# Kernel tuning notes

Hardware: AMD Instinct MI355X
Metric: run time of the kernel (lower is better)

Reference implementation:

```python
import jax, jax.numpy as jnp
import numpy as np

D_MODEL = 96
D_INNER = 192   # ssm_ratio * d_model
R = 6           # dt_rank = ceil(96/16)
DH = 32         # d_inner // dt_rank (per-head dim)
K = 4           # scan directions
N = 16          # d_state
EPS = 1e-5


def setup_inputs() -> dict:
    key = jax.random.key(0)
    ks = jax.random.split(key, 10)
    B, H, W = 8, 64, 64
    f = lambda k, s, sc: jax.random.normal(k, s, jnp.float32) * sc
    return dict(
        x=jax.random.normal(ks[0], (B, H, W, D_MODEL), jnp.float32),
        w_in=f(ks[1], (D_MODEL, D_INNER), 0.02),
        w_conv=f(ks[2], (3, 3, 1, D_INNER), 0.1),      # depthwise HWIO
        b_conv=f(ks[3], (D_INNER,), 0.1),
        x_proj_weight=f(ks[4], (K, R + 2 * N, D_INNER), 0.02),
        A_logs=f(ks[5], (K, R), 0.5),
        Ds=jnp.ones((K, R, DH), jnp.float32),
        dt_bias=0.1 * jax.random.uniform(ks[6], (K, R), jnp.float32),
        ln_g=jnp.ones((D_INNER,), jnp.float32),
        ln_b=jnp.zeros((D_INNER,), jnp.float32),
        w_out=f(ks[7], (D_INNER, D_MODEL), 0.02),
    )


def _cross_scan(x):
    # x: (B,H,W,C) -> (B,L,4,C): [row-major, col-major, rev row, rev col]
    B, H, W, C = x.shape
    x0 = x.reshape(B, H * W, C)
    x1 = jnp.transpose(x, (0, 2, 1, 3)).reshape(B, H * W, C)
    return jnp.stack([x0, x1, x0[:, ::-1], x1[:, ::-1]], axis=2)


def _cross_merge(ys, H, W):
    # ys: (B,L,4,C) -> (B,L,C) summed after undoing each scan order
    B, L, _, C = ys.shape
    y_row = ys[:, :, 0] + ys[:, :, 2][:, ::-1]
    y_col = ys[:, :, 1] + ys[:, :, 3][:, ::-1]
    y_col = jnp.transpose(y_col.reshape(B, W, H, C), (0, 2, 1, 3)).reshape(B, L, C)
    return y_row + y_col


def _selective_scan(us, dts, As, Bs, Cs, Dsr, dtb):
    # us:(B,L,KR,DH) dts:(B,L,KR) As:(KR,) Bs,Cs:(B,L,K,N) Dsr:(KR,DH) dtb:(KR,)
    dt = jax.nn.softplus(dts + dtb)                 # (B,L,KR)
    decay = jnp.exp(dt * As)                        # (B,L,KR)
    xu = dt[..., None] * us                         # (B,L,KR,DH)
    Bh = jnp.repeat(Bs, R, axis=2)                  # (B,L,KR,N) head h -> group h//R
    Ch = jnp.repeat(Cs, R, axis=2)
    B_, L, KR, _ = us.shape
    tfirst = lambda a: jnp.moveaxis(a, 1, 0)

    def step(h, inp):
        dec, xu_t, b_t, c_t = inp                   # (B,KR),(B,KR,DH),(B,KR,N),(B,KR,N)
        h = dec[:, :, None, None] * h + xu_t[..., None] * b_t[:, :, None, :]
        y = jnp.einsum('bkdn,bkn->bkd', h, c_t)
        return h, y

    h0 = jnp.zeros((B_, KR, DH, N), us.dtype)
    _, ys = jax.lax.scan(step, h0, (tfirst(decay), tfirst(xu), tfirst(Bh), tfirst(Ch)))
    ys = jnp.moveaxis(ys, 0, 1)                     # (B,L,KR,DH)
    return ys + us * Dsr                            # skip term D*u


def reference(x, w_in, w_conv, b_conv, x_proj_weight, A_logs, Ds, dt_bias, ln_g, ln_b, w_out):
    B, H, W, _ = x.shape
    L = H * W
    xi = x @ w_in                                   # in_proj (no bias)
    xi = jax.lax.conv_general_dilated(
        xi, w_conv, (1, 1), 'SAME', feature_group_count=D_INNER,
        dimension_numbers=('NHWC', 'HWIO', 'NHWC')) + b_conv
    xi = jax.nn.silu(xi)
    xs = _cross_scan(xi)                            # (B,L,4,D_INNER)
    x_dbl = jnp.einsum('blkd,kcd->blkc', xs, x_proj_weight)
    dts = x_dbl[..., :R].reshape(B, L, K * R)
    Bs = x_dbl[..., R:R + N]                        # (B,L,K,N)
    Cs = x_dbl[..., R + N:]
    us = xs.reshape(B, L, K * R, DH)
    As = -jnp.exp(A_logs.astype(jnp.float32)).reshape(K * R)
    Dsr = Ds.reshape(K * R, DH)
    dtb = dt_bias.reshape(K * R)
    ys = _selective_scan(us, dts, As, Bs, Cs, Dsr, dtb)   # (B,L,KR,DH)
    y = _cross_merge(ys.reshape(B, L, K, R * DH), H, W)   # (B,L,D_INNER)
    mu = y.mean(-1, keepdims=True)
    var = ((y - mu) ** 2).mean(-1, keepdims=True)
    y = (y - mu) / jnp.sqrt(var + EPS) * ln_g + ln_b
    y = y.reshape(B, H, W, D_INNER)
    return y @ w_out                                # out_proj (no bias)
```

## Files before the change

kernel.cpp:

```cpp
#include <hip/hip_runtime.h>
#include <hip/hip_bf16.h>

#define BB 8
#define LL 4096
#define DM 96
#define DI 192
#define RRR 6
#define DHH 32
#define KKK 4
#define NNN 16
#define KRR 24
#define NCH 64
#define TT 64
#define XKC 160

__device__ __forceinline__ float softplus_f(float x){
    float ax = fabsf(x);
    return fmaxf(x, 0.f) + __logf(1.f + __expf(-ax));
}
__device__ __forceinline__ float silu_f(float x){ return x / (1.f + __expf(-x)); }

__device__ __forceinline__ int loc_of(int k, int t){
    int tt = (k >= 2) ? (LL - 1 - t) : t;
    if (k & 1) return ((tt & 63) << 6) | (tt >> 6);
    return tt;
}

__global__ void k0p(const float* __restrict__ W, const float* __restrict__ g,
                    const float* __restrict__ bta, const float* __restrict__ w_out,
                    float* __restrict__ Wp, float* __restrict__ wg, float* __restrict__ sgbw){
    int i = blockIdx.x * 256 + threadIdx.x;
    if (i < DI * XKC){
        int d = i / XKC, kc = i % XKC; int k = kc / 40, nc = kc % 40;
        float v = 0.f;
        if (nc < 6) v = W[(k * 38 + nc) * DI + d];
        else if (nc >= 8) v = W[(k * 38 + (nc - 2)) * DI + d];
        Wp[i] = v;
    } else if (i < DI * XKC + DI * DM){
        int j = i - DI * XKC; int c = j / DM;
        wg[j] = w_out[j] * g[c];
    } else if (i < DI * XKC + DI * DM + DM){
        int m = i - (DI * XKC + DI * DM);
        float s = 0.f, t = 0.f;
        for (int c = 0; c < DI; ++c){
            float w = w_out[c * DM + m];
            s = fmaf(g[c], w, s);
            t = fmaf(bta[c], w, t);
        }
        sgbw[m] = s; sgbw[DM + m] = t;
    }
}

__global__ __launch_bounds__(384) void k1_inproj(const float* __restrict__ x,
                                                 const float* __restrict__ w_in,
                                                 float* __restrict__ xw){
    __shared__ float xT[DM][68];
    int pix0 = blockIdx.x * 64;
    for (int i = threadIdx.x; i < 64 * DM; i += 384){
        int c = i % DM, p = i / DM;
        xT[c][p] = x[(size_t)(pix0 + p) * DM + c];
    }
    __syncthreads();
    int cg = threadIdx.x % 48, pg = threadIdx.x / 48;
    int p0 = pg * 8;
    float4 acc[8];
    #pragma unroll
    for (int i = 0; i < 8; ++i) acc[i] = make_float4(0.f, 0.f, 0.f, 0.f);
    const float* wcol = w_in + cg * 4;
    for (int d = 0; d < DM; ++d){
        float4 w4 = *(const float4*)(wcol + d * DI);
        float4 xa = *(const float4*)(&xT[d][p0]);
        float4 xb = *(const float4*)(&xT[d][p0 + 4]);
        float xs[8] = {xa.x, xa.y, xa.z, xa.w, xb.x, xb.y, xb.z, xb.w};
        #pragma unroll
        for (int pi = 0; pi < 8; ++pi){
            acc[pi].x = fmaf(xs[pi], w4.x, acc[pi].x);
            acc[pi].y = fmaf(xs[pi], w4.y, acc[pi].y);
            acc[pi].z = fmaf(xs[pi], w4.z, acc[pi].z);
            acc[pi].w = fmaf(xs[pi], w4.w, acc[pi].w);
        }
    }
    #pragma unroll
    for (int pi = 0; pi < 8; ++pi)
        *(float4*)(xw + (size_t)(pix0 + p0 + pi) * DI + cg * 4) = acc[pi];
}

__global__ void k2_conv(const float* __restrict__ xw, const float* __restrict__ wc,
                        const float* __restrict__ bc, float* __restrict__ xi){
    int gid = blockIdx.x * 256 + threadIdx.x;
    int c4 = gid % 48; int pix = gid / 48;
    int b = pix >> 12; int l = pix & 4095; int h = l >> 6; int w = l & 63;
    int c = c4 * 4;
    float4 acc = *(const float4*)(bc + c);
    #pragma unroll
    for (int dh = 0; dh < 3; ++dh){
        int hh = h + dh - 1; if ((unsigned)hh >= 64u) continue;
        #pragma unroll
        for (int dw = 0; dw < 3; ++dw){
            int ww2 = w + dw - 1; if ((unsigned)ww2 >= 64u) continue;
            float4 tap = *(const float4*)(xw + (size_t)((b << 12) + (hh << 6) + ww2) * DI + c);
            float4 wv  = *(const float4*)(wc + (dh * 3 + dw) * DI + c);
            acc.x = fmaf(tap.x, wv.x, acc.x);
            acc.y = fmaf(tap.y, wv.y, acc.y);
            acc.z = fmaf(tap.z, wv.z, acc.z);
            acc.w = fmaf(tap.w, wv.w, acc.w);
        }
    }
    acc.x = silu_f(acc.x); acc.y = silu_f(acc.y); acc.z = silu_f(acc.z); acc.w = silu_f(acc.w);
    *(float4*)(xi + (size_t)pix * DI + c) = acc;
}

__global__ __launch_bounds__(320) void k3_proj(const float* __restrict__ xi,
                                               const float* __restrict__ Wp,
                                               float* __restrict__ xdbl){
    __shared__ float xT[DI][68];
    int pix0 = blockIdx.x * 64;
    for (int i = threadIdx.x; i < 64 * DI; i += 320){
        int c = i % DI, p = i / DI;
        xT[c][p] = xi[(size_t)(pix0 + p) * DI + c];
    }
    __syncthreads();
    int kg = threadIdx.x % 40, pg = threadIdx.x / 40;
    int p0 = pg * 8;
    float4 acc[8];
    #pragma unroll
    for (int i = 0; i < 8; ++i) acc[i] = make_float4(0.f, 0.f, 0.f, 0.f);
    const float* wcol = Wp + kg * 4;
    for (int d = 0; d < DI; ++d){
        float4 w4 = *(const float4*)(wcol + d * XKC);
        float4 xa = *(const float4*)(&xT[d][p0]);
        float4 xb = *(const float4*)(&xT[d][p0 + 4]);
        float xs[8] = {xa.x, xa.y, xa.z, xa.w, xb.x, xb.y, xb.z, xb.w};
        #pragma unroll
        for (int pi = 0; pi < 8; ++pi){
            acc[pi].x = fmaf(xs[pi], w4.x, acc[pi].x);
            acc[pi].y = fmaf(xs[pi], w4.y, acc[pi].y);
            acc[pi].z = fmaf(xs[pi], w4.z, acc[pi].z);
            acc[pi].w = fmaf(xs[pi], w4.w, acc[pi].w);
        }
    }
    #pragma unroll
    for (int pi = 0; pi < 8; ++pi)
        *(float4*)(xdbl + (size_t)(pix0 + p0 + pi) * XKC + kg * 4) = acc[pi];
}

__global__ __launch_bounds__(192) void k4a(const float* __restrict__ xi, const float* __restrict__ xdbl,
                    const float* __restrict__ A_logs, const float* __restrict__ dt_bias,
                    float* __restrict__ Pb, float* __restrict__ Sb){
    int chunk = blockIdx.x, k = blockIdx.y, b = blockIdx.z;
    int r = threadIdx.x >> 5, d = threadIdx.x & 31;
    int kr = k * RRR + r;
    float A = -__expf(A_logs[kr]);
    float dtb = dt_bias[kr];
    float h[NNN];
    #pragma unroll
    for (int n = 0; n < NNN; ++n) h[n] = 0.f;
    float P = 1.f;
    const float* xd = xdbl + ((size_t)b << 12) * XKC + k * 40;
    const float* xib = xi + ((size_t)b << 12) * DI + r * DHH + d;
    #pragma unroll 2
    for (int tt = 0; tt < TT; ++tt){
        int t = chunk * TT + tt;
        int loc = loc_of(k, t);
        const float* row = xd + (size_t)loc * XKC;
        float dt = softplus_f(row[r] + dtb);
        float dec = __expf(dt * A);
        float u = xib[(size_t)loc * DI];
        float xu = dt * u;
        P *= dec;
        float Bv[NNN];
        *(float4*)(Bv + 0)  = *(const float4*)(row + 8);
        *(float4*)(Bv + 4)  = *(const float4*)(row + 12);
        *(float4*)(Bv + 8)  = *(const float4*)(row + 16);
        *(float4*)(Bv + 12) = *(const float4*)(row + 20);
        #pragma unroll
        for (int n = 0; n < NNN; ++n) h[n] = fmaf(dec, h[n], xu * Bv[n]);
    }
    size_t sb = (((size_t)(b * KRR + kr) * NCH + chunk) * DHH + d) * NNN;
    #pragma unroll
    for (int n = 0; n < NNN; ++n) Sb[sb + n] = h[n];
    if (d == 0) Pb[(size_t)(b * KRR + kr) * NCH + chunk] = P;
}

__global__ __launch_bounds__(512) void k4b(const float* __restrict__ Pb, float* __restrict__ Sb){
    int scan = blockIdx.x;
    int tid = threadIdx.x;
    size_t base = (size_t)scan * NCH * 512 + tid;
    const float* Pp = Pb + (size_t)scan * NCH;
    float s[NCH];
    #pragma unroll
    for (int c = 0; c < NCH; ++c) s[c] = Sb[base + (size_t)c * 512];
    float hb = 0.f;
    #pragma unroll
    for (int c = 0; c < NCH; ++c){
        float nv = fmaf(Pp[c], hb, s[c]);
        Sb[base + (size_t)c * 512] = hb;
        hb = nv;
    }
}

__global__ __launch_bounds__(192) void k4c(const float* __restrict__ xi, const float* __restrict__ xdbl,
                    const float* __restrict__ A_logs, const float* __restrict__ dt_bias,
                    const float* __restrict__ Ds, const float* __restrict__ Sb,
                    __hip_bfloat16* __restrict__ ybuf){
    int chunk = blockIdx.x, k = blockIdx.y, b = blockIdx.z;
    int r = threadIdx.x >> 5, d = threadIdx.x & 31;
    int kr = k * RRR + r;
    float A = -__expf(A_logs[kr]);
    float dtb = dt_bias[kr];
    float Dv = Ds[kr * DHH + d];
    float h[NNN];
    size_t sb = (((size_t)(b * KRR + kr) * NCH + chunk) * DHH + d) * NNN;
    #pragma unroll
    for (int n = 0; n < NNN; ++n) h[n] = Sb[sb + n];
    const float* xd = xdbl + ((size_t)b << 12) * XKC + k * 40;
    const float* xib = xi + ((size_t)b << 12) * DI + r * DHH + d;
    __hip_bfloat16* yb = ybuf + (size_t)(k * BB + b) * LL * DI + r * DHH + d;
    #pragma unroll 2
    for (int tt = 0; tt < TT; ++tt){
        int t = chunk * TT + tt;
        int loc = loc_of(k, t);
        const float* row = xd + (size_t)loc * XKC;
        float dt = softplus_f(row[r] + dtb);
        float dec = __expf(dt * A);
        float u = xib[(size_t)loc * DI];
        float xu = dt * u;
        float Bv[NNN], Cv[NNN];
        *(float4*)(Bv + 0)  = *(const float4*)(row + 8);
        *(float4*)(Bv + 4)  = *(const float4*)(row + 12);
        *(float4*)(Bv + 8)  = *(const float4*)(row + 16);
        *(float4*)(Bv + 12) = *(const float4*)(row + 20);
        *(float4*)(Cv + 0)  = *(const float4*)(row + 24);
        *(float4*)(Cv + 4)  = *(const float4*)(row + 28);
        *(float4*)(Cv + 8)  = *(const float4*)(row + 32);
        *(float4*)(Cv + 12) = *(const float4*)(row + 36);
        float y = 0.f;
        #pragma unroll
        for (int n = 0; n < NNN; ++n){
            h[n] = fmaf(dec, h[n], xu * Bv[n]);
            y = fmaf(h[n], Cv[n], y);
        }
        y = fmaf(u, Dv, y);
        yb[(size_t)loc * DI] = __float2bfloat16(y);
    }
}

__global__ __launch_bounds__(256) void k5_out(const __hip_bfloat16* __restrict__ ybuf,
                       const float* __restrict__ wg, const float* __restrict__ sgbw,
                       float* __restrict__ out){
    __shared__ float yT[DI][36];
    __shared__ float rsL[32], rmL[32];
    int pix0 = blockIdx.x * 32;
    int b = pix0 >> 12;
    int l0 = pix0 & 4095;
    const size_t kstride = (size_t)BB * LL * DI;
    for (int i = threadIdx.x; i < 32 * DI; i += 256){
        int c = i % DI, p = i / DI;
        size_t off = (size_t)b * LL * DI + (size_t)(l0 + p) * DI + c;
        float s = __bfloat162float(ybuf[off])
                + __bfloat162float(ybuf[off + kstride])
                + __bfloat162float(ybuf[off + 2 * kstride])
                + __bfloat162float(ybuf[off + 3 * kstride]);
        yT[c][p] = s;
    }
    __syncthreads();
    {
        int p = threadIdx.x >> 3, cg = threadIdx.x & 7;
        float s = 0.f, s2 = 0.f;
        for (int c = cg; c < DI; c += 8){ float v = yT[c][p]; s += v; s2 = fmaf(v, v, s2); }
        s += __shfl_xor(s, 1, 64); s2 += __shfl_xor(s2, 1, 64);
        s += __shfl_xor(s, 2, 64); s2 += __shfl_xor(s2, 2, 64);
        s += __shfl_xor(s, 4, 64); s2 += __shfl_xor(s2, 4, 64);
        if (cg == 0){
            float mu = s * (1.f / DI);
            float var = s2 * (1.f / DI) - mu * mu;
            float rs = rsqrtf(var + 1e-5f);
            rsL[p] = rs; rmL[p] = rs * mu;
        }
    }
    __syncthreads();
    if (threadIdx.x < 192){
        int mg = threadIdx.x % 24, pg = threadIdx.x / 24;
        int p0 = pg * 4;
        float4 acc[4];
        #pragma unroll
        for (int i = 0; i < 4; ++i) acc[i] = make_float4(0.f, 0.f, 0.f, 0.f);
        const float* wcol = wg + mg * 4;
        for (int c = 0; c < DI; ++c){
            float4 w4 = *(const float4*)(wcol + c * DM);
            float4 yv = *(const float4*)(&yT[c][p0]);
            float ys[4] = {yv.x, yv.y, yv.z, yv.w};
            #pragma unroll
            for (int pi = 0; pi < 4; ++pi){
                acc[pi].x = fmaf(ys[pi], w4.x, acc[pi].x);
                acc[pi].y = fmaf(ys[pi], w4.y, acc[pi].y);
                acc[pi].z = fmaf(ys[pi], w4.z, acc[pi].z);
                acc[pi].w = fmaf(ys[pi], w4.w, acc[pi].w);
            }
        }
        float4 sg4 = *(const float4*)(sgbw + mg * 4);
        float4 bw4 = *(const float4*)(sgbw + DM + mg * 4);
        #pragma unroll
        for (int pi = 0; pi < 4; ++pi){
            float rs = rsL[p0 + pi], rm = rmL[p0 + pi];
            float4 o;
            o.x = fmaf(acc[pi].x, rs, fmaf(-rm, sg4.x, bw4.x));
            o.y = fmaf(acc[pi].y, rs, fmaf(-rm, sg4.y, bw4.y));
            o.z = fmaf(acc[pi].z, rs, fmaf(-rm, sg4.z, bw4.z));
            o.w = fmaf(acc[pi].w, rs, fmaf(-rm, sg4.w, bw4.w));
            *(float4*)(out + (size_t)(pix0 + p0 + pi) * DM + mg * 4) = o;
        }
    }
}

extern "C" void kernel_launch(void* const* d_in, const int* in_sizes, int n_in,
                              void* d_out, int out_size, void* d_ws, size_t ws_size,
                              hipStream_t stream){
    const float* x      = (const float*)d_in[0];
    const float* w_in   = (const float*)d_in[1];
    const float* w_conv = (const float*)d_in[2];
    const float* b_conv = (const float*)d_in[3];
    const float* xproj  = (const float*)d_in[4];
    const float* A_logs = (const float*)d_in[5];
    const float* Ds     = (const float*)d_in[6];
    const float* dtbias = (const float*)d_in[7];
    const float* ln_g   = (const float*)d_in[8];
    const float* ln_b   = (const float*)d_in[9];
    const float* w_out  = (const float*)d_in[10];
    float* out = (float*)d_out;

    float* ws   = (float*)d_ws;
    float* xi   = ws;
    float* xdbl = xi + 6291456;
    float* Pb   = xdbl + 5242880;
    float* Sb   = Pb + 16384;
    float* Wp   = Sb + 6291456;
    float* wg   = Wp + 30720;
    float* sgbw = wg + 18432;
    float* big  = sgbw + 192;
    float* xw   = big;
    __hip_bfloat16* ybuf = (__hip_bfloat16*)big;

    k0p<<<193, 256, 0, stream>>>(xproj, ln_g, ln_b, w_out, Wp, wg, sgbw);
    k1_inproj<<<512, 384, 0, stream>>>(x, w_in, xw);
    k2_conv<<<6144, 256, 0, stream>>>(xw, w_conv, b_conv, xi);
    k3_proj<<<512, 320, 0, stream>>>(xi, Wp, xdbl);
    k4a<<<dim3(NCH, KKK, BB), 192, 0, stream>>>(xi, xdbl, A_logs, dtbias, Pb, Sb);
    k4b<<<192, 512, 0, stream>>>(Pb, Sb);
    k4c<<<dim3(NCH, KKK, BB), 192, 0, stream>>>(xi, xdbl, A_logs, dtbias, Ds, Sb, ybuf);
    k5_out<<<1024, 256, 0, stream>>>(ybuf, wg, sgbw, out);
}
```

Baseline: 304.7 us.

## Lay out scan inputs in per-direction sequence order and precompute dt/decay

The conv kernel now also writes a transposed copy of the activations, so column-major directions can be read contiguously. The projection kernel writes per-direction records in scan order and precomputes softplus(dt) and exp(dt*A) once, instead of in both scan passes. The scan kernels then stream through the records and activations with linear strides and no index remapping, and the merge undoes the orderings when reading. In exchange there is an extra full activation write and a larger workspace.

```diff
diff --git a/kernel.cpp b/kernel.cpp
--- a/kernel.cpp
+++ b/kernel.cpp
@@ -12,7 +12,7 @@
 #define KRR 24
 #define NCH 64
 #define TT 64
-#define XKC 160
+#define RST 48
 
 __device__ __forceinline__ float softplus_f(float x){
     float ax = fabsf(x);
@@ -20,27 +20,22 @@
 }
 __device__ __forceinline__ float silu_f(float x){ return x / (1.f + __expf(-x)); }
 
-__device__ __forceinline__ int loc_of(int k, int t){
-    int tt = (k >= 2) ? (LL - 1 - t) : t;
-    if (k & 1) return ((tt & 63) << 6) | (tt >> 6);
-    return tt;
-}
-
 __global__ void k0p(const float* __restrict__ W, const float* __restrict__ g,
                     const float* __restrict__ bta, const float* __restrict__ w_out,
-                    float* __restrict__ Wp, float* __restrict__ wg, float* __restrict__ sgbw){
+                    float* __restrict__ WpR, float* __restrict__ wg, float* __restrict__ sgbw){
     int i = blockIdx.x * 256 + threadIdx.x;
-    if (i < DI * XKC){
-        int d = i / XKC, kc = i % XKC; int k = kc / 40, nc = kc % 40;
+    if (i < DI * 160){
+        int d = i / 160, cc = i % 160; int gq = cc / 40, nc = cc % 40;
+        int dir = (gq == 0) ? 0 : (gq == 1) ? 2 : (gq == 2) ? 1 : 3;
         float v = 0.f;
-        if (nc < 6) v = W[(k * 38 + nc) * DI + d];
-        else if (nc >= 8) v = W[(k * 38 + (nc - 2)) * DI + d];
-        Wp[i] = v;
-    } else if (i < DI * XKC + DI * DM){
-        int j = i - DI * XKC; int c = j / DM;
+        if (nc < 6) v = W[(dir * 38 + nc) * DI + d];
+        else if (nc >= 8) v = W[(dir * 38 + (nc - 2)) * DI + d];
+        WpR[i] = v;
+    } else if (i < DI * 160 + DI * DM){
+        int j = i - DI * 160; int c = j / DM;
         wg[j] = w_out[j] * g[c];
-    } else if (i < DI * XKC + DI * DM + DM){
-        int m = i - (DI * XKC + DI * DM);
+    } else if (i < DI * 160 + DI * DM + DM){
+        int m = i - (DI * 160 + DI * DM);
         float s = 0.f, t = 0.f;
         for (int c = 0; c < DI; ++c){
             float w = w_out[c * DM + m];
@@ -86,7 +81,8 @@
 }
 
 __global__ void k2_conv(const float* __restrict__ xw, const float* __restrict__ wc,
-                        const float* __restrict__ bc, float* __restrict__ xi){
+                        const float* __restrict__ bc, float* __restrict__ xi,
+                        float* __restrict__ xiT){
     int gid = blockIdx.x * 256 + threadIdx.x;
     int c4 = gid % 48; int pix = gid / 48;
     int b = pix >> 12; int l = pix & 4095; int h = l >> 6; int w = l & 63;
@@ -108,73 +104,114 @@
     }
     acc.x = silu_f(acc.x); acc.y = silu_f(acc.y); acc.z = silu_f(acc.z); acc.w = silu_f(acc.w);
     *(float4*)(xi + (size_t)pix * DI + c) = acc;
-}
-
-__global__ __launch_bounds__(320) void k3_proj(const float* __restrict__ xi,
-                                               const float* __restrict__ Wp,
-                                               float* __restrict__ xdbl){
-    __shared__ float xT[DI][68];
-    int pix0 = blockIdx.x * 64;
+    int lT = ((l & 63) << 6) | (l >> 6);
+    *(float4*)(xiT + (size_t)((b << 12) + lT) * DI + c) = acc;
+}
+
+__global__ __launch_bounds__(320) void k3seq(const float* __restrict__ xi,
+                                             const float* __restrict__ xiT,
+                                             const float* __restrict__ WpR,
+                                             const float* __restrict__ A_logs,
+                                             const float* __restrict__ dtb,
+                                             float* __restrict__ rec){
+    __shared__ float xT[DI][65];
+    int pass = blockIdx.y, b = blockIdx.z;
+    const float* src = (pass ? xiT : xi) + (((size_t)b) << 12) * DI;
+    int p0blk = blockIdx.x * 64;
     for (int i = threadIdx.x; i < 64 * DI; i += 320){
         int c = i % DI, p = i / DI;
-        xT[c][p] = xi[(size_t)(pix0 + p) * DI + c];
+        xT[c][p] = src[(size_t)(p0blk + p) * DI + c];
     }
     __syncthreads();
-    int kg = threadIdx.x % 40, pg = threadIdx.x / 40;
-    int p0 = pg * 8;
-    float4 acc[8];
-    #pragma unroll
-    for (int i = 0; i < 8; ++i) acc[i] = make_float4(0.f, 0.f, 0.f, 0.f);
-    const float* wcol = Wp + kg * 4;
+    int kg = threadIdx.x % 20, pg = threadIdx.x / 20;
+    int p0 = pg * 4;
+    float4 acc[4];
+    #pragma unroll
+    for (int i = 0; i < 4; ++i) acc[i] = make_float4(0.f, 0.f, 0.f, 0.f);
+    const float* wcol = WpR + pass * 80 + kg * 4;
     for (int d = 0; d < DI; ++d){
-        float4 w4 = *(const float4*)(wcol + d * XKC);
-        float4 xa = *(const float4*)(&xT[d][p0]);
-        float4 xb = *(const float4*)(&xT[d][p0 + 4]);
-        float xs[8] = {xa.x, xa.y, xa.z, xa.w, xb.x, xb.y, xb.z, xb.w};
-        #pragma unroll
-        for (int pi = 0; pi < 8; ++pi){
+        float4 w4 = *(const float4*)(wcol + d * 160);
+        float4 xv = *(const float4*)(&xT[d][p0]);
+        float xs[4] = {xv.x, xv.y, xv.z, xv.w};
+        #pragma unroll
+        for (int pi = 0; pi < 4; ++pi){
             acc[pi].x = fmaf(xs[pi], w4.x, acc[pi].x);
             acc[pi].y = fmaf(xs[pi], w4.y, acc[pi].y);
             acc[pi].z = fmaf(xs[pi], w4.z, acc[pi].z);
             acc[pi].w = fmaf(xs[pi], w4.w, acc[pi].w);
         }
     }
-    #pragma unroll
-    for (int pi = 0; pi < 8; ++pi)
-        *(float4*)(xdbl + (size_t)(pix0 + p0 + pi) * XKC + kg * 4) = acc[pi];
-}
-
-__global__ __launch_bounds__(192) void k4a(const float* __restrict__ xi, const float* __restrict__ xdbl,
-                    const float* __restrict__ A_logs, const float* __restrict__ dt_bias,
-                    float* __restrict__ Pb, float* __restrict__ Sb){
+    int gq = kg / 10;
+    int dir = (pass == 0) ? (gq == 0 ? 0 : 2) : (gq == 0 ? 1 : 3);
+    int nc0 = (kg % 10) * 4;
+    float* rb = rec + (size_t)(b * KKK + dir) * LL * RST;
+    float A0, A1, A2, A3, b0, b1, b2, b3;
+    if (nc0 == 0){
+        A0 = -__expf(A_logs[dir * RRR + 0]); b0 = dtb[dir * RRR + 0];
+        A1 = -__expf(A_logs[dir * RRR + 1]); b1 = dtb[dir * RRR + 1];
+        A2 = -__expf(A_logs[dir * RRR + 2]); b2 = dtb[dir * RRR + 2];
+        A3 = -__expf(A_logs[dir * RRR + 3]); b3 = dtb[dir * RRR + 3];
+    } else if (nc0 == 4){
+        A0 = -__expf(A_logs[dir * RRR + 4]); b0 = dtb[dir * RRR + 4];
+        A1 = -__expf(A_logs[dir * RRR + 5]); b1 = dtb[dir * RRR + 5];
+    }
+    #pragma unroll
+    for (int pi = 0; pi < 4; ++pi){
+        int gp = p0blk + p0 + pi;
+        int t = (dir < 2) ? gp : (LL - 1 - gp);
+        float* rw = rb + (size_t)t * RST;
+        float4 v = acc[pi];
+        if (nc0 == 0){
+            float4 dt4, dc4;
+            dt4.x = softplus_f(v.x + b0); dc4.x = __expf(dt4.x * A0);
+            dt4.y = softplus_f(v.y + b1); dc4.y = __expf(dt4.y * A1);
+            dt4.z = softplus_f(v.z + b2); dc4.z = __expf(dt4.z * A2);
+            dt4.w = softplus_f(v.w + b3); dc4.w = __expf(dt4.w * A3);
+            *(float4*)(rw + 0) = dt4;
+            *(float4*)(rw + 8) = dc4;
+        } else if (nc0 == 4){
+            float4 dt4, dc4;
+            dt4.x = softplus_f(v.x + b0); dc4.x = __expf(dt4.x * A0);
+            dt4.y = softplus_f(v.y + b1); dc4.y = __expf(dt4.y * A1);
+            dt4.z = 0.f; dt4.w = 0.f; dc4.z = 0.f; dc4.w = 0.f;
+            *(float4*)(rw + 4)  = dt4;
+            *(float4*)(rw + 12) = dc4;
+        } else {
+            *(float4*)(rw + nc0 + 8) = v;
+        }
+    }
+}
+
+__global__ __launch_bounds__(192) void k4a(const float* __restrict__ xi, const float* __restrict__ xiT,
+                                           const float* __restrict__ rec,
+                                           float* __restrict__ Pb, float* __restrict__ Sb){
     int chunk = blockIdx.x, k = blockIdx.y, b = blockIdx.z;
     int r = threadIdx.x >> 5, d = threadIdx.x & 31;
     int kr = k * RRR + r;
-    float A = -__expf(A_logs[kr]);
-    float dtb = dt_bias[kr];
+    const float* rp = rec + ((size_t)(b * KKK + k) * LL + chunk * TT) * RST;
+    const float* xb = ((k & 1) ? xiT : xi) + (((size_t)b) << 12) * DI + r * DHH + d;
+    const float* up; ptrdiff_t ust;
+    if (k < 2){ up = xb + (size_t)(chunk * TT) * DI;          ust = DI;  }
+    else      { up = xb + (size_t)(LL - 1 - chunk * TT) * DI; ust = -(ptrdiff_t)DI; }
     float h[NNN];
     #pragma unroll
     for (int n = 0; n < NNN; ++n) h[n] = 0.f;
     float P = 1.f;
-    const float* xd = xdbl + ((size_t)b << 12) * XKC + k * 40;
-    const float* xib = xi + ((size_t)b << 12) * DI + r * DHH + d;
-    #pragma unroll 2
+    #pragma unroll 4
     for (int tt = 0; tt < TT; ++tt){
-        int t = chunk * TT + tt;
-        int loc = loc_of(k, t);
-        const float* row = xd + (size_t)loc * XKC;
-        float dt = softplus_f(row[r] + dtb);
-        float dec = __expf(dt * A);
-        float u = xib[(size_t)loc * DI];
+        float dt  = rp[r];
+        float dec = rp[8 + r];
+        float u = *up;
         float xu = dt * u;
         P *= dec;
         float Bv[NNN];
-        *(float4*)(Bv + 0)  = *(const float4*)(row + 8);
-        *(float4*)(Bv + 4)  = *(const float4*)(row + 12);
-        *(float4*)(Bv + 8)  = *(const float4*)(row + 16);
-        *(float4*)(Bv + 12) = *(const float4*)(row + 20);
+        *(float4*)(Bv + 0)  = *(const float4*)(rp + 16);
+        *(float4*)(Bv + 4)  = *(const float4*)(rp + 20);
+        *(float4*)(Bv + 8)  = *(const float4*)(rp + 24);
+        *(float4*)(Bv + 12) = *(const float4*)(rp + 28);
         #pragma unroll
         for (int n = 0; n < NNN; ++n) h[n] = fmaf(dec, h[n], xu * Bv[n]);
+        rp += RST; up += ust;
     }
     size_t sb = (((size_t)(b * KRR + kr) * NCH + chunk) * DHH + d) * NNN;
     #pragma unroll
@@ -199,41 +236,39 @@
     }
 }
 
-__global__ __launch_bounds__(192) void k4c(const float* __restrict__ xi, const float* __restrict__ xdbl,
-                    const float* __restrict__ A_logs, const float* __restrict__ dt_bias,
-                    const float* __restrict__ Ds, const float* __restrict__ Sb,
-                    __hip_bfloat16* __restrict__ ybuf){
+__global__ __launch_bounds__(192) void k4c(const float* __restrict__ xi, const float* __restrict__ xiT,
+                                           const float* __restrict__ rec,
+                                           const float* __restrict__ Ds, const float* __restrict__ Sb,
+                                           __hip_bfloat16* __restrict__ ybuf){
     int chunk = blockIdx.x, k = blockIdx.y, b = blockIdx.z;
     int r = threadIdx.x >> 5, d = threadIdx.x & 31;
     int kr = k * RRR + r;
-    float A = -__expf(A_logs[kr]);
-    float dtb = dt_bias[kr];
     float Dv = Ds[kr * DHH + d];
     float h[NNN];
     size_t sb = (((size_t)(b * KRR + kr) * NCH + chunk) * DHH + d) * NNN;
     #pragma unroll
     for (int n = 0; n < NNN; ++n) h[n] = Sb[sb + n];
-    const float* xd = xdbl + ((size_t)b << 12) * XKC + k * 40;
-    const float* xib = xi + ((size_t)b << 12) * DI + r * DHH + d;
-    __hip_bfloat16* yb = ybuf + (size_t)(k * BB + b) * LL * DI + r * DHH + d;
+    const float* rp = rec + ((size_t)(b * KKK + k) * LL + chunk * TT) * RST;
+    const float* xb = ((k & 1) ? xiT : xi) + (((size_t)b) << 12) * DI + r * DHH + d;
+    const float* up; ptrdiff_t ust;
+    if (k < 2){ up = xb + (size_t)(chunk * TT) * DI;          ust = DI;  }
+    else      { up = xb + (size_t)(LL - 1 - chunk * TT) * DI; ust = -(ptrdiff_t)DI; }
+    __hip_bfloat16* yp = ybuf + ((size_t)(k * BB + b) * LL + chunk * TT) * DI + r * DHH + d;
     #pragma unroll 2
     for (int tt = 0; tt < TT; ++tt){
-        int t = chunk * TT + tt;
-        int loc = loc_of(k, t);
-        const float* row = xd + (size_t)loc * XKC;
-        float dt = softplus_f(row[r] + dtb);
-        float dec = __expf(dt * A);
-        float u = xib[(size_t)loc * DI];
+        float dt  = rp[r];
+        float dec = rp[8 + r];
+        float u = *up;
         float xu = dt * u;
         float Bv[NNN], Cv[NNN];
-        *(float4*)(Bv + 0)  = *(const float4*)(row + 8);
-        *(float4*)(Bv + 4)  = *(const float4*)(row + 12);
-        *(float4*)(Bv + 8)  = *(const float4*)(row + 16);
-        *(float4*)(Bv + 12) = *(const float4*)(row + 20);
-        *(float4*)(Cv + 0)  = *(const float4*)(row + 24);
-        *(float4*)(Cv + 4)  = *(const float4*)(row + 28);
-        *(float4*)(Cv + 8)  = *(const float4*)(row + 32);
-        *(float4*)(Cv + 12) = *(const float4*)(row + 36);
+        *(float4*)(Bv + 0)  = *(const float4*)(rp + 16);
+        *(float4*)(Bv + 4)  = *(const float4*)(rp + 20);
+        *(float4*)(Bv + 8)  = *(const float4*)(rp + 24);
+        *(float4*)(Bv + 12) = *(const float4*)(rp + 28);
+        *(float4*)(Cv + 0)  = *(const float4*)(rp + 32);
+        *(float4*)(Cv + 4)  = *(const float4*)(rp + 36);
+        *(float4*)(Cv + 8)  = *(const float4*)(rp + 40);
+        *(float4*)(Cv + 12) = *(const float4*)(rp + 44);
         float y = 0.f;
         #pragma unroll
         for (int n = 0; n < NNN; ++n){
@@ -241,7 +276,8 @@
             y = fmaf(h[n], Cv[n], y);
         }
         y = fmaf(u, Dv, y);
-        yb[(size_t)loc * DI] = __float2bfloat16(y);
+        *yp = __float2bfloat16(y);
+        rp += RST; up += ust; yp += DI;
     }
 }
 
@@ -253,14 +289,18 @@
     int pix0 = blockIdx.x * 32;
     int b = pix0 >> 12;
     int l0 = pix0 & 4095;
-    const size_t kstride = (size_t)BB * LL * DI;
+    const __hip_bfloat16* y0 = ybuf + (size_t)(0 * BB + b) * LL * DI;
+    const __hip_bfloat16* y1 = ybuf + (size_t)(1 * BB + b) * LL * DI;
+    const __hip_bfloat16* y2 = ybuf + (size_t)(2 * BB + b) * LL * DI;
+    const __hip_bfloat16* y3 = ybuf + (size_t)(3 * BB + b) * LL * DI;
     for (int i = threadIdx.x; i < 32 * DI; i += 256){
         int c = i % DI, p = i / DI;
-        size_t off = (size_t)b * LL * DI + (size_t)(l0 + p) * DI + c;
-        float s = __bfloat162float(ybuf[off])
-                + __bfloat162float(ybuf[off + kstride])
-                + __bfloat162float(ybuf[off + 2 * kstride])
-                + __bfloat162float(ybuf[off + 3 * kstride]);
+        int l = l0 + p; int hh = l >> 6, ww = l & 63;
+        int lT = (ww << 6) | hh;
+        float s = __bfloat162float(y0[(size_t)l * DI + c])
+                + __bfloat162float(y2[(size_t)(LL - 1 - l) * DI + c])
+                + __bfloat162float(y1[(size_t)lT * DI + c])
+                + __bfloat162float(y3[(size_t)(LL - 1 - lT) * DI + c]);
         yT[c][p] = s;
     }
     __syncthreads();
@@ -331,22 +371,23 @@
 
     float* ws   = (float*)d_ws;
     float* xi   = ws;
-    float* xdbl = xi + 6291456;
-    float* Pb   = xdbl + 5242880;
-    float* Sb   = Pb + 16384;
-    float* Wp   = Sb + 6291456;
-    float* wg   = Wp + 30720;
+    float* xiT  = xi + 6291456;
+    float* Sb   = xiT + 6291456;
+    float* Pb   = Sb + 6291456;
+    float* WpR  = Pb + 16384;
+    float* wg   = WpR + 30720;
     float* sgbw = wg + 18432;
     float* big  = sgbw + 192;
     float* xw   = big;
-    __hip_bfloat16* ybuf = (__hip_bfloat16*)big;
-
-    k0p<<<193, 256, 0, stream>>>(xproj, ln_g, ln_b, w_out, Wp, wg, sgbw);
+    float* rec  = big;
+    __hip_bfloat16* ybuf = (__hip_bfloat16*)(big + 6291456);
+
+    k0p<<<193, 256, 0, stream>>>(xproj, ln_g, ln_b, w_out, WpR, wg, sgbw);
     k1_inproj<<<512, 384, 0, stream>>>(x, w_in, xw);
-    k2_conv<<<6144, 256, 0, stream>>>(xw, w_conv, b_conv, xi);
-    k3_proj<<<512, 320, 0, stream>>>(xi, Wp, xdbl);
-    k4a<<<dim3(NCH, KKK, BB), 192, 0, stream>>>(xi, xdbl, A_logs, dtbias, Pb, Sb);
+    k2_conv<<<6144, 256, 0, stream>>>(xw, w_conv, b_conv, xi, xiT);
+    k3seq<<<dim3(64, 2, BB), 320, 0, stream>>>(xi, xiT, WpR, A_logs, dtbias, rec);
+    k4a<<<dim3(NCH, KKK, BB), 192, 0, stream>>>(xi, xiT, rec, Pb, Sb);
     k4b<<<192, 512, 0, stream>>>(Pb, Sb);
-    k4c<<<dim3(NCH, KKK, BB), 192, 0, stream>>>(xi, xdbl, A_logs, dtbias, Ds, Sb, ybuf);
+    k4c<<<dim3(NCH, KKK, BB), 192, 0, stream>>>(xi, xiT, rec, Ds, Sb, ybuf);
     k5_out<<<1024, 256, 0, stream>>>(ybuf, wg, sgbw, out);
 }
```

Result: no change. 308.4 us (+1.2%).
